# Kernel tuning notes

Hardware: AMD Instinct MI355X
Metric: run time of the kernel (lower is better)

Reference implementation:

```python
import jax, jax.numpy as jnp
import numpy as np

N_NODES = 100000
N_EDGES = 1600000  # undirected edges (each pair listed once, no self loops)
IN_CH, HID, OUT_CH = 512, 64, 32
MU, P, K = 0.1, 1.5, 2
EPS = 1e-8


def setup_inputs() -> dict:
    key = jax.random.key(0)
    k_x, k_src, k_off, k_w1, k_w2 = jax.random.split(key, 5)
    x = jax.random.normal(k_x, (N_NODES, IN_CH), dtype=jnp.float32)
    # undirected edge list with no self loops: dst = (src + offset) % N, offset in [1, N)
    src = jax.random.randint(k_src, (N_EDGES,), 0, N_NODES)
    off = jax.random.randint(k_off, (N_EDGES,), 1, N_NODES)
    dst = (src + off) % N_NODES
    edge_index = jnp.stack([src, dst], axis=0)
    # parameters (lin1 of pGNNNet, lin1 of pGNNConv)
    W1 = jax.random.normal(k_w1, (IN_CH, HID), dtype=jnp.float32) / np.sqrt(IN_CH)
    b1 = jnp.zeros((HID,), dtype=jnp.float32)
    W2 = jax.random.normal(k_w2, (HID, OUT_CH), dtype=jnp.float32) / np.sqrt(HID)
    b2 = jnp.zeros((OUT_CH,), dtype=jnp.float32)
    return {"x": x, "edge_index": edge_index, "W1": W1, "b1": b1, "W2": W2, "b2": b2}


def reference(x, edge_index, W1, b1, W2, b2):
    src, dst = edge_index[0], edge_index[1]
    n = x.shape[0]
    # pGNNNet.lin1 + ReLU (dropout is identity in eval mode)
    h = jax.nn.relu(x @ W1 + b1)                   # [N, HID]
    # pGNNConv.lin1 applied before propagation
    f = h @ W2 + b2                                # [N, OUT]
    # degrees of the symmetric adjacency (no self loops)
    ones = jnp.ones(src.shape, dtype=f.dtype)
    deg = jax.ops.segment_sum(ones, src, num_segments=n) + \
          jax.ops.segment_sum(ones, dst, num_segments=n)
    dinv = jnp.where(deg > 0, 1.0 / deg, 0.0)      # [N]
    dis = jnp.sqrt(dinv)                           # D^{-1/2}
    out = f
    for _ in range(K):
        gs = out * dis[:, None]                    # D^{-1/2} f
        g = gs[src] - gs[dst]                      # graph gradient per edge [E, OUT]
        # edge reweighting: ||grad||^{p-2}
        w = jnp.power(jnp.sum(g * g, axis=1) + EPS, (P - 2.0) * 0.5)   # [E]
        # row sums of M (symmetric, M_ij = w_e)
        s = jax.ops.segment_sum(w, src, num_segments=n) + \
            jax.ops.segment_sum(w, dst, num_segments=n)
        alpha = 1.0 / (s * dinv + MU)              # [N]
        beta = MU * alpha
        # (D^{-1/2} M D^{-1/2} out): scatter-add messages both directions
        m = w[:, None]
        agg = jax.ops.segment_sum(m * gs[dst], src, num_segments=n) + \
              jax.ops.segment_sum(m * gs[src], dst, num_segments=n)
        out = alpha[:, None] * (dis[:, None] * agg) + beta[:, None] * f
    return jax.nn.log_softmax(out, axis=1)
```

## Files before the change

### kernel.cpp

```cpp
#include <hip/hip_runtime.h>
#include <hip/hip_bf16.h>
#include <math.h>

#define N_NODES 100000
#define N_EDGES 1600000
#define IN_CH 512
#define HID 64
#define OUT_CH 32
#define MU 0.1f
#define EPS 1e-8f

#define HE (2 * N_EDGES)
#define ABLK 625
#define EPT 20
#define NBUCK 391
#define PCAP 10240

typedef short bf16x8 __attribute__((ext_vector_type(8)));
typedef unsigned short us8 __attribute__((ext_vector_type(8)));
typedef float f32x4 __attribute__((ext_vector_type(4)));

__device__ __forceinline__ short f2bf(float f) {
  __hip_bfloat16 h = __float2bfloat16(f);
  return *reinterpret_cast<short*>(&h);
}
__device__ __forceinline__ float bf2f(unsigned short u) {
  unsigned int b = ((unsigned int)u) << 16;
  return __uint_as_float(b);
}

__global__ __launch_bounds__(256) void k_bcount(
    const int* __restrict__ ends, int* __restrict__ bcnt,
    const float* __restrict__ W1, const float* __restrict__ W2,
    short* __restrict__ w1t, short* __restrict__ w2t) {
  const int t = threadIdx.x;
  const int b = blockIdx.x;
  {
    const int i = b * 256 + t;
    if (i < IN_CH * HID) {
      int k = i / HID, c = i % HID;
      w1t[c * IN_CH + k] = f2bf(W1[i]);
    } else if (i < IN_CH * HID + HID * OUT_CH) {
      int j = i - IN_CH * HID;
      w2t[(j % OUT_CH) * HID + (j / OUT_CH)] = f2bf(W2[j]);
    }
  }
  __shared__ int cnt[NBUCK];
  for (int i = t; i < NBUCK; i += 256) cnt[i] = 0;
  __syncthreads();
  const int base = b * (256 * EPT);
  #pragma unroll
  for (int j = 0; j < EPT; ++j) {
    int u = ends[base + j * 256 + t];
    atomicAdd(&cnt[u >> 8], 1);
  }
  __syncthreads();
  for (int i = t; i < NBUCK; i += 256) bcnt[i * ABLK + b] = cnt[i];
}

__global__ __launch_bounds__(256) void k_rowsum(const int* __restrict__ bcnt,
                                                int* __restrict__ btotal) {
  const int b = blockIdx.x;
  int s = 0;
  for (int i = threadIdx.x; i < ABLK; i += 256) s += bcnt[b * ABLK + i];
  #pragma unroll
  for (int k = 1; k < 64; k <<= 1) s += __shfl_xor(s, k);
  __shared__ int ws[4];
  if ((threadIdx.x & 63) == 0) ws[threadIdx.x >> 6] = s;
  __syncthreads();
  if (threadIdx.x == 0) btotal[b] = ws[0] + ws[1] + ws[2] + ws[3];
}

__global__ __launch_bounds__(256) void k_colscan(const int* __restrict__ bcnt,
                                                 const int* __restrict__ btotal,
                                                 int* __restrict__ bucketbase,
                                                 int* __restrict__ sbase) {
  __shared__ int sh[256];
  __shared__ int ws[4];
  const int b = blockIdx.x;
  const int t = threadIdx.x;
  int pre = 0;
  for (int i = t; i < b; i += 256) pre += btotal[i];
  #pragma unroll
  for (int k = 1; k < 64; k <<= 1) pre += __shfl_xor(pre, k);
  if ((t & 63) == 0) ws[t >> 6] = pre;
  __syncthreads();
  int carry = ws[0] + ws[1] + ws[2] + ws[3];
  if (t == 0) bucketbase[b] = carry;
  for (int c = 0; c < ABLK; c += 256) {
    const int idx = c + t;
    int v = idx < ABLK ? bcnt[b * ABLK + idx] : 0;
    sh[t] = v;
    __syncthreads();
    for (int s = 1; s < 256; s <<= 1) {
      int a = t >= s ? sh[t - s] : 0;
      __syncthreads();
      sh[t] += a;
      __syncthreads();
    }
    if (idx < ABLK) sbase[idx * NBUCK + b] = carry + sh[t] - v;
    carry += sh[255];
    __syncthreads();
  }
}

__global__ __launch_bounds__(256) void k_bscatter(const int* __restrict__ ends,
                                                  const int* __restrict__ sbase,
                                                  int* __restrict__ pairs) {
  __shared__ int cur[NBUCK];
  for (int i = threadIdx.x; i < NBUCK; i += 256)
    cur[i] = sbase[blockIdx.x * NBUCK + i];
  __syncthreads();
  const int base = blockIdx.x * (256 * EPT);
  #pragma unroll
  for (int j = 0; j < EPT; ++j) {
    const int i = base + j * 256 + threadIdx.x;
    const int u = ends[i];
    const int nb = ends[i < N_EDGES ? i + N_EDGES : i - N_EDGES];
    const int slot = atomicAdd(&cur[u >> 8], 1);
    pairs[slot] = ((u & 255) << 24) | nb;
  }
}

__global__ __launch_bounds__(256) void k_csr(const int* __restrict__ pairs,
                                             const int* __restrict__ bucketbase,
                                             const int* __restrict__ btotal,
                                             int2* __restrict__ degrs,
                                             int* __restrict__ adj) {
  __shared__ int pl[PCAP];
  __shared__ int cnt[256];
  __shared__ int sh[256];
  const int b = blockIdx.x, t = threadIdx.x;
  const int pbase = bucketbase[b];
  const int psz = btotal[b];
  const bool fits = psz <= PCAP;
  cnt[t] = 0;
  __syncthreads();
  if (fits) {
    for (int i = t; i < psz; i += 256) {
      int p = pairs[pbase + i];
      pl[i] = p;
      atomicAdd(&cnt[((unsigned)p) >> 24], 1);
    }
  } else {
    for (int i = t; i < psz; i += 256)
      atomicAdd(&cnt[((unsigned)pairs[pbase + i]) >> 24], 1);
  }
  __syncthreads();
  const int d = cnt[t];
  sh[t] = d;
  __syncthreads();
  for (int s = 1; s < 256; s <<= 1) {
    int a = t >= s ? sh[t - s] : 0;
    __syncthreads();
    sh[t] += a;
    __syncthreads();
  }
  const int rs = pbase + sh[t] - d;
  const int v = (b << 8) + t;
  if (v < N_NODES) degrs[v] = make_int2(d, rs);
  __syncthreads();
  cnt[t] = rs;
  __syncthreads();
  for (int i = t; i < psz; i += 256) {
    const int p = fits ? pl[i] : pairs[pbase + i];
    adj[atomicAdd(&cnt[((unsigned)p) >> 24], 1)] = p & 0xFFFFFF;
  }
}

__global__ __launch_bounds__(256, 2) void k_mlp(
    const float* __restrict__ x, const short* __restrict__ w1t,
    const float* __restrict__ b1, const short* __restrict__ w2t,
    const float* __restrict__ b2, const int2* __restrict__ degrs,
    float* __restrict__ f, unsigned short* __restrict__ gs) {
  __shared__ short ht[4][16][72];

  const int t = threadIdx.x;
  const int w = t >> 6;
  const int l = t & 63;
  const int lr = l & 15;
  const int kq = l >> 4;

  const int band = blockIdx.x * 64 + w * 16;
  const int gr = band + lr;
  const int grl = gr < N_NODES ? gr : N_NODES - 1;
  const float* xrow = x + (size_t)grl * IN_CH + kq * 8;

  f32x4 xa[32];
  #pragma unroll
  for (int ksub = 0; ksub < 16; ++ksub) {
    xa[2 * ksub] = *(const f32x4*)(xrow + ksub * 32);
    xa[2 * ksub + 1] = *(const f32x4*)(xrow + ksub * 32 + 4);
  }

  f32x4 acc1[4] = {};
  #pragma unroll
  for (int ksub = 0; ksub < 16; ++ksub) {
    const f32x4 alo = xa[2 * ksub];
    const f32x4 ahi = xa[2 * ksub + 1];
    bf16x8 a;
    a[0] = f2bf(alo[0]); a[1] = f2bf(alo[1]); a[2] = f2bf(alo[2]); a[3] = f2bf(alo[3]);
    a[4] = f2bf(ahi[0]); a[5] = f2bf(ahi[1]); a[6] = f2bf(ahi[2]); a[7] = f2bf(ahi[3]);
    #pragma unroll
    for (int ct = 0; ct < 4; ++ct) {
      const int c = ct * 16 + lr;
      bf16x8 bfrag = *(const bf16x8*)&w1t[c * IN_CH + ksub * 32 + kq * 8];
      acc1[ct] = __builtin_amdgcn_mfma_f32_16x16x32_bf16(a, bfrag, acc1[ct], 0, 0, 0);
    }
  }

  #pragma unroll
  for (int ct = 0; ct < 4; ++ct) {
    const int c = ct * 16 + lr;
    const float bb = b1[c];
    #pragma unroll
    for (int r = 0; r < 4; ++r) {
      float h = acc1[ct][r] + bb;
      ht[w][kq * 4 + r][c] = f2bf(h > 0.f ? h : 0.f);
    }
  }
  __syncthreads();

  f32x4 acc2[2] = {};
  #pragma unroll
  for (int ks = 0; ks < 2; ++ks) {
    bf16x8 a2 = *(const bf16x8*)&ht[w][lr][ks * 32 + kq * 8];
    #pragma unroll
    for (int ct = 0; ct < 2; ++ct) {
      const int c = ct * 16 + lr;
      bf16x8 bfrag = *(const bf16x8*)&w2t[c * HID + ks * 32 + kq * 8];
      acc2[ct] = __builtin_amdgcn_mfma_f32_16x16x32_bf16(a2, bfrag, acc2[ct], 0, 0, 0);
    }
  }

  #pragma unroll
  for (int r = 0; r < 4; ++r) {
    const int gr2 = band + kq * 4 + r;
    if (gr2 < N_NODES) {
      const int d = degrs[gr2].x;
      const float di = d > 0 ? 1.0f / (float)d : 0.0f;
      const float disv = sqrtf(di);
      #pragma unroll
      for (int ct = 0; ct < 2; ++ct) {
        const int c = ct * 16 + lr;
        const float fv = acc2[ct][r] + b2[c];
        f[(size_t)gr2 * OUT_CH + c] = fv;
        gs[(size_t)gr2 * OUT_CH + c] = (unsigned short)f2bf(fv * disv);
      }
    }
  }
}

template <bool FINAL>
__global__ __launch_bounds__(256) void k_prop(
    const unsigned short* __restrict__ gs_in, const float* __restrict__ f,
    const int2* __restrict__ degrs, const int* __restrict__ adj,
    float* __restrict__ outf, unsigned short* __restrict__ outg) {
  const int v = blockIdx.x * 4 + (threadIdx.x >> 6);
  const int lane = threadIdx.x & 63;
  const int slot = lane >> 2;
  const int cg2 = (lane & 3) << 3;

  const int2 dr = degrs[v];
  const int dg = dr.x;
  const int i0 = dr.y;
  const us8 gvu = *(const us8*)&gs_in[v * OUT_CH + cg2];
  const float4 fv0 = *(const float4*)&f[v * OUT_CH + cg2];
  const float4 fv1 = *(const float4*)&f[v * OUT_CH + cg2 + 4];
  float gv[8];
  #pragma unroll
  for (int j = 0; j < 8; ++j) gv[j] = bf2f(gvu[j]);

  const float dinvv = dg > 0 ? 1.0f / (float)dg : 0.0f;
  const float disv = sqrtf(dinvv);

  float accs = 0.f;
  float acca[8] = {0.f, 0.f, 0.f, 0.f, 0.f, 0.f, 0.f, 0.f};

  int u[3];
  #pragma unroll
  for (int q = 0; q < 3; ++q) {
    const int idx = q * 16 + slot;
    u[q] = idx < dg ? adj[i0 + idx] : v;
  }
  us8 guu[3];
  #pragma unroll
  for (int q = 0; q < 3; ++q)
    guu[q] = *(const us8*)&gs_in[u[q] * OUT_CH + cg2];
  #pragma unroll
  for (int q = 0; q < 3; ++q) {
    const bool vq = (q * 16 + slot) < dg;
    float gu[8];
    #pragma unroll
    for (int j = 0; j < 8; ++j) gu[j] = bf2f(guu[q][j]);
    float d = gv[0] - gu[0];
    float sq = d * d;
    #pragma unroll
    for (int j = 1; j < 8; ++j) { d = gv[j] - gu[j]; sq = fmaf(d, d, sq); }
    sq += __shfl_xor(sq, 1);
    sq += __shfl_xor(sq, 2);
    const float wq = vq ? __frsqrt_rn(sqrtf(sq + EPS)) : 0.f;
    accs += wq;
    #pragma unroll
    for (int j = 0; j < 8; ++j) acca[j] = fmaf(wq, gu[j], acca[j]);
  }
  for (int base = 48; base < dg; base += 16) {
    const int idx = base + slot;
    const bool vq = idx < dg;
    const int ut = vq ? adj[i0 + idx] : v;
    const us8 gut = *(const us8*)&gs_in[ut * OUT_CH + cg2];
    float gu[8];
    #pragma unroll
    for (int j = 0; j < 8; ++j) gu[j] = bf2f(gut[j]);
    float d = gv[0] - gu[0];
    float sq = d * d;
    #pragma unroll
    for (int j = 1; j < 8; ++j) { d = gv[j] - gu[j]; sq = fmaf(d, d, sq); }
    sq += __shfl_xor(sq, 1);
    sq += __shfl_xor(sq, 2);
    const float wq = vq ? __frsqrt_rn(sqrtf(sq + EPS)) : 0.f;
    accs += wq;
    #pragma unroll
    for (int j = 0; j < 8; ++j) acca[j] = fmaf(wq, gu[j], acca[j]);
  }

  #pragma unroll
  for (int s = 4; s <= 32; s <<= 1) {
    accs += __shfl_xor(accs, s);
    #pragma unroll
    for (int j = 0; j < 8; ++j) acca[j] += __shfl_xor(acca[j], s);
  }

  const float alpha = 1.0f / (accs * dinvv + MU);
  const float ad = alpha * disv;
  const float ba = MU * alpha;
  float r[8];
  r[0] = fmaf(ad, acca[0], ba * fv0.x);
  r[1] = fmaf(ad, acca[1], ba * fv0.y);
  r[2] = fmaf(ad, acca[2], ba * fv0.z);
  r[3] = fmaf(ad, acca[3], ba * fv0.w);
  r[4] = fmaf(ad, acca[4], ba * fv1.x);
  r[5] = fmaf(ad, acca[5], ba * fv1.y);
  r[6] = fmaf(ad, acca[6], ba * fv1.z);
  r[7] = fmaf(ad, acca[7], ba * fv1.w);

  if (FINAL) {
    float m = r[0];
    #pragma unroll
    for (int j = 1; j < 8; ++j) m = fmaxf(m, r[j]);
    m = fmaxf(m, __shfl_xor(m, 1));
    m = fmaxf(m, __shfl_xor(m, 2));
    float se = 0.f;
    #pragma unroll
    for (int j = 0; j < 8; ++j) se += __expf(r[j] - m);
    se += __shfl_xor(se, 1);
    se += __shfl_xor(se, 2);
    const float lse = m + __logf(se);
    if (slot == 0) {
      float4 o0 = make_float4(r[0] - lse, r[1] - lse, r[2] - lse, r[3] - lse);
      float4 o1 = make_float4(r[4] - lse, r[5] - lse, r[6] - lse, r[7] - lse);
      *(float4*)&outf[v * OUT_CH + cg2] = o0;
      *(float4*)&outf[v * OUT_CH + cg2 + 4] = o1;
    }
  } else {
    if (slot == 0) {
      us8 o;
      #pragma unroll
      for (int j = 0; j < 8; ++j) o[j] = (unsigned short)f2bf(r[j] * disv);
      *(us8*)&outg[v * OUT_CH + cg2] = o;
    }
  }
}

extern "C" void kernel_launch(void* const* d_in, const int* in_sizes, int n_in,
                              void* d_out, int out_size, void* d_ws, size_t ws_size,
                              hipStream_t stream) {
  const float* x = (const float*)d_in[0];
  const int* ei = (const int*)d_in[1];
  const float* W1 = (const float*)d_in[2];
  const float* b1 = (const float*)d_in[3];
  const float* W2 = (const float*)d_in[4];
  const float* b2 = (const float*)d_in[5];
  float* out = (float*)d_out;

  float* f = (float*)d_ws;
  unsigned short* gsa = (unsigned short*)(f + (size_t)N_NODES * 32);
  unsigned short* gsb = gsa + (size_t)N_NODES * 32;
  int2* degrs = (int2*)(gsb + (size_t)N_NODES * 32);
  int* adj = (int*)(degrs + N_NODES);
  short* w1t = (short*)(adj + 2 * N_EDGES);
  short* w2t = w1t + IN_CH * HID;
  int* bcnt = (int*)(w2t + HID * OUT_CH);
  int* sbase = bcnt + NBUCK * ABLK;
  int* btotal = sbase + NBUCK * ABLK;
  int* bucketbase = btotal + NBUCK + 1;
  int* pairs = (int*)f;

  k_bcount<<<ABLK, 256, 0, stream>>>(ei, bcnt, W1, W2, w1t, w2t);
  k_rowsum<<<NBUCK, 256, 0, stream>>>(bcnt, btotal);
  k_colscan<<<NBUCK, 256, 0, stream>>>(bcnt, btotal, bucketbase, sbase);
  k_bscatter<<<ABLK, 256, 0, stream>>>(ei, sbase, pairs);
  k_csr<<<NBUCK, 256, 0, stream>>>(pairs, bucketbase, btotal, degrs, adj);
  k_mlp<<<(N_NODES + 63) / 64, 256, 0, stream>>>(x, w1t, b1, w2t, b2, degrs, f, gsa);
  k_prop<false><<<N_NODES / 4, 256, 0, stream>>>(gsa, f, degrs, adj, nullptr, gsb);
  k_prop<true><<<N_NODES / 4, 256, 0, stream>>>(gsb, f, degrs, adj, out, nullptr);
}
```

Before: 266.1 us.

## Replace count-scan-scatter bucketing with fixed-capacity atomic buckets; tune MLP occupancy

The three-pass bucket sort (per-block counts, row sums, column scan) plus a separate scatter is collapsed into one kernel. Each bucket gets a fixed-capacity region of BCAP slots, and each block reserves its slots with a global atomicAdd on a per-bucket cursor that is memset to zero first. This removes two kernel launches and the scan traffic, at the cost of padded buckets, a nondeterministic neighbour order and a capacity assumption that holds only for near-uniform degree distributions. Separately, the MLP kernel loads x in two halves to cut register pressure and raises its launch bounds to 3 blocks per CU.

After: 264.0 us. No clear change (-0.8%).

```diff
diff --git a/kernel.cpp b/kernel.cpp
--- a/kernel.cpp
+++ b/kernel.cpp
@@ -14,6 +14,7 @@
 #define ABLK 625
 #define EPT 20
 #define NBUCK 391
+#define BCAP 9216
 #define PCAP 10240
 
 typedef short bf16x8 __attribute__((ext_vector_type(8)));
@@ -29,10 +30,10 @@
   return __uint_as_float(b);
 }
 
-__global__ __launch_bounds__(256) void k_bcount(
-    const int* __restrict__ ends, int* __restrict__ bcnt,
-    const float* __restrict__ W1, const float* __restrict__ W2,
-    short* __restrict__ w1t, short* __restrict__ w2t) {
+__global__ __launch_bounds__(256) void k_scatter(
+    const int* __restrict__ ends, const float* __restrict__ W1,
+    const float* __restrict__ W2, short* __restrict__ w1t,
+    short* __restrict__ w2t, int* __restrict__ gcur, int* __restrict__ pairs) {
   const int t = threadIdx.x;
   const int b = blockIdx.x;
   {
@@ -49,90 +50,36 @@
   for (int i = t; i < NBUCK; i += 256) cnt[i] = 0;
   __syncthreads();
   const int base = b * (256 * EPT);
+  int us[EPT];
+  #pragma unroll
+  for (int j = 0; j < EPT; ++j) us[j] = ends[base + j * 256 + t];
+  #pragma unroll
+  for (int j = 0; j < EPT; ++j) atomicAdd(&cnt[us[j] >> 8], 1);
+  __syncthreads();
+  for (int i = t; i < NBUCK; i += 256) {
+    const int c = cnt[i];
+    cnt[i] = c > 0 ? i * BCAP + atomicAdd(&gcur[i], c) : 0;
+  }
+  __syncthreads();
   #pragma unroll
   for (int j = 0; j < EPT; ++j) {
-    int u = ends[base + j * 256 + t];
-    atomicAdd(&cnt[u >> 8], 1);
-  }
-  __syncthreads();
-  for (int i = t; i < NBUCK; i += 256) bcnt[i * ABLK + b] = cnt[i];
-}
-
-__global__ __launch_bounds__(256) void k_rowsum(const int* __restrict__ bcnt,
-                                                int* __restrict__ btotal) {
-  const int b = blockIdx.x;
-  int s = 0;
-  for (int i = threadIdx.x; i < ABLK; i += 256) s += bcnt[b * ABLK + i];
-  #pragma unroll
-  for (int k = 1; k < 64; k <<= 1) s += __shfl_xor(s, k);
-  __shared__ int ws[4];
-  if ((threadIdx.x & 63) == 0) ws[threadIdx.x >> 6] = s;
-  __syncthreads();
-  if (threadIdx.x == 0) btotal[b] = ws[0] + ws[1] + ws[2] + ws[3];
-}
-
-__global__ __launch_bounds__(256) void k_colscan(const int* __restrict__ bcnt,
-                                                 const int* __restrict__ btotal,
-                                                 int* __restrict__ bucketbase,
-                                                 int* __restrict__ sbase) {
-  __shared__ int sh[256];
-  __shared__ int ws[4];
-  const int b = blockIdx.x;
-  const int t = threadIdx.x;
-  int pre = 0;
-  for (int i = t; i < b; i += 256) pre += btotal[i];
-  #pragma unroll
-  for (int k = 1; k < 64; k <<= 1) pre += __shfl_xor(pre, k);
-  if ((t & 63) == 0) ws[t >> 6] = pre;
-  __syncthreads();
-  int carry = ws[0] + ws[1] + ws[2] + ws[3];
-  if (t == 0) bucketbase[b] = carry;
-  for (int c = 0; c < ABLK; c += 256) {
-    const int idx = c + t;
-    int v = idx < ABLK ? bcnt[b * ABLK + idx] : 0;
-    sh[t] = v;
-    __syncthreads();
-    for (int s = 1; s < 256; s <<= 1) {
-      int a = t >= s ? sh[t - s] : 0;
-      __syncthreads();
-      sh[t] += a;
-      __syncthreads();
-    }
-    if (idx < ABLK) sbase[idx * NBUCK + b] = carry + sh[t] - v;
-    carry += sh[255];
-    __syncthreads();
-  }
-}
-
-__global__ __launch_bounds__(256) void k_bscatter(const int* __restrict__ ends,
-                                                  const int* __restrict__ sbase,
-                                                  int* __restrict__ pairs) {
-  __shared__ int cur[NBUCK];
-  for (int i = threadIdx.x; i < NBUCK; i += 256)
-    cur[i] = sbase[blockIdx.x * NBUCK + i];
-  __syncthreads();
-  const int base = blockIdx.x * (256 * EPT);
-  #pragma unroll
-  for (int j = 0; j < EPT; ++j) {
-    const int i = base + j * 256 + threadIdx.x;
-    const int u = ends[i];
+    const int i = base + j * 256 + t;
+    const int u = us[j];
     const int nb = ends[i < N_EDGES ? i + N_EDGES : i - N_EDGES];
-    const int slot = atomicAdd(&cur[u >> 8], 1);
-    pairs[slot] = ((u & 255) << 24) | nb;
+    pairs[atomicAdd(&cnt[u >> 8], 1)] = ((u & 255) << 24) | nb;
   }
 }
 
 __global__ __launch_bounds__(256) void k_csr(const int* __restrict__ pairs,
-                                             const int* __restrict__ bucketbase,
-                                             const int* __restrict__ btotal,
+                                             const int* __restrict__ gcur,
                                              int2* __restrict__ degrs,
                                              int* __restrict__ adj) {
   __shared__ int pl[PCAP];
   __shared__ int cnt[256];
   __shared__ int sh[256];
   const int b = blockIdx.x, t = threadIdx.x;
-  const int pbase = bucketbase[b];
-  const int psz = btotal[b];
+  const int pbase = b * BCAP;
+  const int psz = gcur[b];
   const bool fits = psz <= PCAP;
   cnt[t] = 0;
   __syncthreads();
@@ -168,7 +115,7 @@
   }
 }
 
-__global__ __launch_bounds__(256, 2) void k_mlp(
+__global__ __launch_bounds__(256, 3) void k_mlp(
     const float* __restrict__ x, const short* __restrict__ w1t,
     const float* __restrict__ b1, const short* __restrict__ w2t,
     const float* __restrict__ b2, const int2* __restrict__ degrs,
@@ -186,25 +133,46 @@
   const int grl = gr < N_NODES ? gr : N_NODES - 1;
   const float* xrow = x + (size_t)grl * IN_CH + kq * 8;
 
-  f32x4 xa[32];
-  #pragma unroll
-  for (int ksub = 0; ksub < 16; ++ksub) {
-    xa[2 * ksub] = *(const f32x4*)(xrow + ksub * 32);
-    xa[2 * ksub + 1] = *(const f32x4*)(xrow + ksub * 32 + 4);
-  }
-
+  f32x4 xa[16];
+  #pragma unroll
+  for (int s = 0; s < 8; ++s) {
+    xa[2 * s] = *(const f32x4*)(xrow + s * 32);
+    xa[2 * s + 1] = *(const f32x4*)(xrow + s * 32 + 4);
+  }
+  bf16x8 af[8];
+  #pragma unroll
+  for (int s = 0; s < 8; ++s) {
+    af[s][0] = f2bf(xa[2 * s][0]); af[s][1] = f2bf(xa[2 * s][1]);
+    af[s][2] = f2bf(xa[2 * s][2]); af[s][3] = f2bf(xa[2 * s][3]);
+    af[s][4] = f2bf(xa[2 * s + 1][0]); af[s][5] = f2bf(xa[2 * s + 1][1]);
+    af[s][6] = f2bf(xa[2 * s + 1][2]); af[s][7] = f2bf(xa[2 * s + 1][3]);
+  }
+  #pragma unroll
+  for (int s = 0; s < 8; ++s) {
+    xa[2 * s] = *(const f32x4*)(xrow + (s + 8) * 32);
+    xa[2 * s + 1] = *(const f32x4*)(xrow + (s + 8) * 32 + 4);
+  }
   f32x4 acc1[4] = {};
   #pragma unroll
-  for (int ksub = 0; ksub < 16; ++ksub) {
-    const f32x4 alo = xa[2 * ksub];
-    const f32x4 ahi = xa[2 * ksub + 1];
-    bf16x8 a;
-    a[0] = f2bf(alo[0]); a[1] = f2bf(alo[1]); a[2] = f2bf(alo[2]); a[3] = f2bf(alo[3]);
-    a[4] = f2bf(ahi[0]); a[5] = f2bf(ahi[1]); a[6] = f2bf(ahi[2]); a[7] = f2bf(ahi[3]);
+  for (int s = 0; s < 8; ++s) {
     #pragma unroll
     for (int ct = 0; ct < 4; ++ct) {
       const int c = ct * 16 + lr;
-      bf16x8 bfrag = *(const bf16x8*)&w1t[c * IN_CH + ksub * 32 + kq * 8];
+      bf16x8 bfrag = *(const bf16x8*)&w1t[c * IN_CH + s * 32 + kq * 8];
+      acc1[ct] = __builtin_amdgcn_mfma_f32_16x16x32_bf16(af[s], bfrag, acc1[ct], 0, 0, 0);
+    }
+  }
+  #pragma unroll
+  for (int s = 0; s < 8; ++s) {
+    bf16x8 a;
+    a[0] = f2bf(xa[2 * s][0]); a[1] = f2bf(xa[2 * s][1]);
+    a[2] = f2bf(xa[2 * s][2]); a[3] = f2bf(xa[2 * s][3]);
+    a[4] = f2bf(xa[2 * s + 1][0]); a[5] = f2bf(xa[2 * s + 1][1]);
+    a[6] = f2bf(xa[2 * s + 1][2]); a[7] = f2bf(xa[2 * s + 1][3]);
+    #pragma unroll
+    for (int ct = 0; ct < 4; ++ct) {
+      const int c = ct * 16 + lr;
+      bf16x8 bfrag = *(const bf16x8*)&w1t[c * IN_CH + (s + 8) * 32 + kq * 8];
       acc1[ct] = __builtin_amdgcn_mfma_f32_16x16x32_bf16(a, bfrag, acc1[ct], 0, 0, 0);
     }
   }
@@ -388,19 +356,14 @@
   unsigned short* gsb = gsa + (size_t)N_NODES * 32;
   int2* degrs = (int2*)(gsb + (size_t)N_NODES * 32);
   int* adj = (int*)(degrs + N_NODES);
-  short* w1t = (short*)(adj + 2 * N_EDGES);
+  short* w1t = (short*)(adj + NBUCK * BCAP);
   short* w2t = w1t + IN_CH * HID;
-  int* bcnt = (int*)(w2t + HID * OUT_CH);
-  int* sbase = bcnt + NBUCK * ABLK;
-  int* btotal = sbase + NBUCK * ABLK;
-  int* bucketbase = btotal + NBUCK + 1;
+  int* gcur = (int*)(w2t + HID * OUT_CH);
   int* pairs = (int*)f;
 
-  k_bcount<<<ABLK, 256, 0, stream>>>(ei, bcnt, W1, W2, w1t, w2t);
-  k_rowsum<<<NBUCK, 256, 0, stream>>>(bcnt, btotal);
-  k_colscan<<<NBUCK, 256, 0, stream>>>(bcnt, btotal, bucketbase, sbase);
-  k_bscatter<<<ABLK, 256, 0, stream>>>(ei, sbase, pairs);
-  k_csr<<<NBUCK, 256, 0, stream>>>(pairs, bucketbase, btotal, degrs, adj);
+  hipMemsetAsync(gcur, 0, NBUCK * sizeof(int), stream);
+  k_scatter<<<ABLK, 256, 0, stream>>>(ei, W1, W2, w1t, w2t, gcur, pairs);
+  k_csr<<<NBUCK, 256, 0, stream>>>(pairs, gcur, degrs, adj);
   k_mlp<<<(N_NODES + 63) / 64, 256, 0, stream>>>(x, w1t, b1, w2t, b2, degrs, f, gsa);
   k_prop<false><<<N_NODES / 4, 256, 0, stream>>>(gsa, f, degrs, adj, nullptr, gsb);
   k_prop<true><<<N_NODES / 4, 256, 0, stream>>>(gsb, f, degrs, adj, out, nullptr);
```
